# Kernel tuning notes

Measured on AMD Instinct MI355X. Metric: run time of the kernel, lower is better.

## Reference

```python
import jax, jax.numpy as jnp
import numpy as np

N = 50000        # n nodes (cells)
C = 1024         # common genes
H = 128          # edge_h_dim
HG = 128         # edge_hidden
E = 1600000      # edges (avg degree 32)
LAYERS = 2       # gnn_layers (unset in original __init__; fixed here)
EPS = 1e-8


def setup_inputs() -> dict:
    key = jax.random.key(0)
    ks = jax.random.split(key, 10)
    x_common = jax.random.normal(ks[0], (N, C), dtype=jnp.float32)
    src = jax.random.randint(ks[1], (E,), 0, N, dtype=jnp.int32)
    dst = jax.random.randint(ks[2], (E,), 0, N, dtype=jnp.int32)
    base_w = jax.random.uniform(ks[3], (E,), dtype=jnp.float32)
    # encoder params: Linear(C,H) -> ReLU -> Linear(H,H) -> ReLU
    W1 = jax.random.normal(ks[4], (C, H), dtype=jnp.float32) * 0.02
    b1 = jnp.zeros((H,), dtype=jnp.float32)
    W2 = jax.random.normal(ks[5], (H, H), dtype=jnp.float32) * 0.1
    b2 = jnp.zeros((H,), dtype=jnp.float32)
    # edge gate params: Linear(2H, HG) -> ReLU -> Linear(HG, 1)
    Wg1 = jax.random.normal(ks[6], (2 * H, HG), dtype=jnp.float32) * 0.1
    bg1 = jnp.zeros((HG,), dtype=jnp.float32)
    Wg2 = jax.random.normal(ks[7], (HG, 1), dtype=jnp.float32) * 0.1
    bg2 = jnp.full((1,), 2.0, dtype=jnp.float32)  # original init: bias=2.0
    # node reliability logits
    rho_raw = jax.random.normal(ks[8], (N,), dtype=jnp.float32) * 0.5
    return dict(x_common=x_common, src=src, dst=dst, base_w=base_w,
                W1=W1, b1=b1, W2=W2, b2=b2,
                Wg1=Wg1, bg1=bg1, Wg2=Wg2, bg2=bg2, rho_raw=rho_raw)


def reference(x_common, src, dst, base_w, W1, b1, W2, b2, Wg1, bg1, Wg2, bg2, rho_raw):
    # enc: [N, C] -> [N, H]
    h = jax.nn.relu(jax.nn.relu(x_common @ W1 + b1) @ W2 + b2)
    rho = jax.nn.sigmoid(rho_raw)                 # [N]
    rr = rho[src] * rho[dst]                      # [E] per-edge reliability factor
    for _ in range(LAYERS):
        h_src = h[src]                            # [E, H] gather
        h_dst = h[dst]                            # [E, H] gather
        z = jnp.concatenate([h_src, h_dst], axis=1)               # [E, 2H]
        gate = jax.nn.sigmoid(jax.nn.relu(z @ Wg1 + bg1) @ Wg2 + bg2)[:, 0]  # [E]
        w = base_w * gate * rr                    # [E]
        m = jax.ops.segment_sum(w[:, None] * h_src, dst, num_segments=N)     # [N, H]
        deg = jax.ops.segment_sum(w, dst, num_segments=N)                    # [N]
        h = m / (deg[:, None] + EPS)
    return h
```

## Files before the change

### kernel.cpp

```cpp
#include <hip/hip_runtime.h>
#include <stdint.h>

#define NN 50000
#define CC 1024
#define HH 128
#define EE 1600000
#define EPSV 1e-8f
#define NSTRIPE 8
#define STRIPE_N 6250
#define NBUCK (NN*NSTRIPE)
#define SCAN_BLKS 1563

typedef __attribute__((ext_vector_type(8))) short bf16x8;
typedef __attribute__((ext_vector_type(4))) float f32x4;
typedef __attribute__((ext_vector_type(2))) float f32x2;

__device__ __forceinline__ unsigned short f32_to_bf16(float f){
  union { float f; uint32_t u; } cv; cv.f = f;
  uint32_t u = cv.u;
  return (unsigned short)((u + 0x7FFFu + ((u >> 16) & 1u)) >> 16);
}
__device__ __forceinline__ float bf16lo_to_f32(uint32_t w){
  union { uint32_t u; float f; } cv; cv.u = w << 16; return cv.f;
}
__device__ __forceinline__ float bf16hi_to_f32(uint32_t w){
  union { uint32_t u; float f; } cv; cv.u = w & 0xFFFF0000u; return cv.f;
}

#define DPP_ADD(x, ctrl) ((x) + __int_as_float(__builtin_amdgcn_update_dpp(0, __float_as_int(x), (ctrl), 0xF, 0xF, true)))

#define GLOAD_LDS16(g, l) __builtin_amdgcn_global_load_lds( \
    (const __attribute__((address_space(1))) uint32_t*)(g), \
    (__attribute__((address_space(3))) uint32_t*)(l), 16, 0, 0)


__global__ __launch_bounds__(256) void k_prep_all(
    const float* __restrict__ W1, const float* __restrict__ W2,
    const float* __restrict__ Wg1,
    unsigned short* __restrict__ W1T, unsigned short* __restrict__ W2T,
    unsigned short* __restrict__ Wg1T){
  int idx = blockIdx.x*256 + threadIdx.x;
  if(idx < 131072){
    int n = idx >> 10, k = idx & 1023;
    W1T[idx] = f32_to_bf16(W1[k*128 + n]);
  } else if(idx < 131072 + 16384){
    int i = idx - 131072;
    int n = i >> 7, k = i & 127;
    W2T[i] = f32_to_bf16(W2[k*128 + n]);
  } else if(idx < 131072 + 16384 + 32768){
    int i = idx - 131072 - 16384;
    int c = i >> 7, k = i & 127;
    int row = (c < 128) ? k : (128 + k);
    int col = (c < 128) ? c : (c - 128);
    Wg1T[i] = f32_to_bf16(Wg1[row*128 + col]);
  }
}


__global__ __launch_bounds__(256) void k_hist(const int* __restrict__ src,
    const int* __restrict__ dst, int* __restrict__ counts,
    int* __restrict__ rank){
  int e = blockIdx.x*256 + threadIdx.x;
  if(e >= EE) return;
  int key = dst[e]*NSTRIPE + (int)((unsigned)src[e] / STRIPE_N);
  rank[e] = atomicAdd(&counts[key], 1);
}

__global__ __launch_bounds__(256) void k_scan1(const int* __restrict__ counts,
    int* __restrict__ lexcl, int* __restrict__ bsum){
  __shared__ int buf[256];
  const int t = threadIdx.x, i = blockIdx.x*256 + t;
  int v = (i < NBUCK) ? counts[i] : 0;
  buf[t] = v;
  __syncthreads();
  for(int off = 1; off < 256; off <<= 1){
    int add = (t >= off) ? buf[t-off] : 0;
    __syncthreads();
    buf[t] += add;
    __syncthreads();
  }
  if(i < NBUCK) lexcl[i] = buf[t] - v;
  if(t == 255) bsum[blockIdx.x] = buf[255];
}

__global__ __launch_bounds__(1024) void k_scan_mid(const int* __restrict__ bsum,
    int* __restrict__ bexcl){
  __shared__ int buf[1024];
  __shared__ int carry_s;
  const int t = threadIdx.x;
  if(t == 0) carry_s = 0;
  __syncthreads();
  for(int base = 0; base < SCAN_BLKS; base += 1024){
    int v = (base+t < SCAN_BLKS) ? bsum[base+t] : 0;
    buf[t] = v;
    __syncthreads();
    for(int off = 1; off < 1024; off <<= 1){
      int add = (t >= off) ? buf[t-off] : 0;
      __syncthreads();
      buf[t] += add;
      __syncthreads();
    }
    int carry = carry_s;
    if(base+t < SCAN_BLKS) bexcl[base+t] = carry + buf[t] - v;
    __syncthreads();
    if(t == 1023) carry_s = carry + buf[1023];
    __syncthreads();
  }
}

__global__ __launch_bounds__(256) void k_scan3(const int* __restrict__ lexcl,
    const int* __restrict__ bexcl, int* __restrict__ bptr){
  const int i = blockIdx.x*256 + threadIdx.x;
  if(i < NBUCK) bptr[i] = lexcl[i] + bexcl[blockIdx.x];
  if(i == 0) bptr[NBUCK] = EE;
}

__global__ __launch_bounds__(256) void k_fill(const int* __restrict__ src,
    const int* __restrict__ dst, const float* __restrict__ base_w,
    const float* __restrict__ rho_raw, const int* __restrict__ bptr,
    const int* __restrict__ rank, float2* __restrict__ scp){
  int e = blockIdx.x*256 + threadIdx.x;
  if(e >= EE) return;
  int s = src[e], d = dst[e];
  int key = d*NSTRIPE + (int)((unsigned)s / STRIPE_N);
  int p = bptr[key] + rank[e];
  float rs = 1.f/(1.f + __expf(-rho_raw[s]));
  float rd = 1.f/(1.f + __expf(-rho_raw[d]));
  scp[p] = make_float2(base_w[e]*rs*rd, __int_as_float(s));
}


__global__ __launch_bounds__(256) void k_enc1(
    const float* __restrict__ X, const unsigned short* __restrict__ W1T,
    const float* __restrict__ b1, unsigned short* __restrict__ h1)
{
  __shared__ __attribute__((aligned(16))) float          Af[2][64*32];
  __shared__ __attribute__((aligned(16))) unsigned short Bf[2][128*32];

  const int t = threadIdx.x, w = t >> 6, lane = t & 63;
  const int rowL = lane & 15, kq = lane >> 4;
  const int wm = w >> 1, wn = w & 1;
  const int row0 = blockIdx.x * 64;

  const int a_rl0 = w*16 + (lane >> 3);
  const int a_cl  = lane & 7;
  int agr0 = row0 + a_rl0;     if(agr0 >= NN) agr0 = NN-1;
  int agr1 = row0 + a_rl0 + 8; if(agr1 >= NN) agr1 = NN-1;
  const float* a_src0 = X + (size_t)agr0*1024 + (a_cl ^ (a_rl0 & 7))*4;
  const float* a_src1 = X + (size_t)agr1*1024 + (a_cl ^ ((a_rl0+8) & 7))*4;
  const int b_rl0 = w*32 + (lane >> 2);
  const int b_cl  = lane & 3;
  const int bkey0 = (b_rl0 ^ (b_rl0 >> 2)) & 3;
  const int bkey1 = ((b_rl0+16) ^ ((b_rl0+16) >> 2)) & 3;
  const unsigned short* b_src0 = W1T + (size_t)b_rl0*1024 + (b_cl ^ bkey0)*8;
  const unsigned short* b_src1 = W1T + (size_t)(b_rl0+16)*1024 + (b_cl ^ bkey1)*8;

  #define STAGE(buf, k0)  do{                                              \
    GLOAD_LDS16(a_src0 + (k0), &Af[buf][(w*16    )*32]);                   \
    GLOAD_LDS16(a_src1 + (k0), &Af[buf][(w*16 + 8)*32]);                   \
    GLOAD_LDS16(b_src0 + (k0), &Bf[buf][(w*32     )*32]);                  \
    GLOAD_LDS16(b_src1 + (k0), &Bf[buf][(w*32 + 16)*32]);                  \
  }while(0)

  f32x4 acc[2][4] = {};
  const int arow0 = wm*32 + rowL;
  const int akey  = rowL & 7;
  const int bkeyR = (rowL ^ (rowL >> 2)) & 3;

  auto COMPUTE = [&](const float* afb, const unsigned short* bfb){
    bf16x8 af[2];
    #pragma unroll
    for(int mf = 0; mf < 2; mf++){
      const int ar = arow0 + mf*16;
      f32x4 x0 = *(const f32x4*)&afb[ar*32 + (((2*kq  ) ^ akey) << 2)];
      f32x4 x1 = *(const f32x4*)&afb[ar*32 + (((2*kq+1) ^ akey) << 2)];
      union { bf16x8 v; unsigned short s[8]; } pk;
      #pragma unroll
      for(int j = 0; j < 4; j++){ pk.s[j] = f32_to_bf16(x0[j]); pk.s[4+j] = f32_to_bf16(x1[j]); }
      af[mf] = pk.v;
    }
    bf16x8 bfr[4];
    #pragma unroll
    for(int nf = 0; nf < 4; nf++){
      const int br = wn*64 + nf*16 + rowL;
      bfr[nf] = *(const bf16x8*)&bfb[br*32 + ((kq ^ bkeyR) << 3)];
    }
    #pragma unroll
    for(int mf = 0; mf < 2; mf++)
      #pragma unroll
      for(int nf = 0; nf < 4; nf++)
        acc[mf][nf] = __builtin_amdgcn_mfma_f32_16x16x32_bf16(af[mf], bfr[nf], acc[mf][nf], 0, 0, 0);
  };

  #define STEP(cbuf, sbuf, sk)  do{                                        \
    STAGE(sbuf, (sk)*32);                                                  \
    asm volatile("s_waitcnt vmcnt(4)" ::: "memory");                       \
    __builtin_amdgcn_s_barrier();                                          \
    __builtin_amdgcn_sched_barrier(0);                                     \
    COMPUTE(&Af[cbuf][0], &Bf[cbuf][0]);                                   \
    __builtin_amdgcn_s_barrier();                                          \
  }while(0)

  STAGE(0, 0);
  for(int tt = 0; tt < 30; tt += 2){
    STEP(0, 1, tt + 1);
    STEP(1, 0, tt + 2);
  }
  STEP(0, 1, 31);
  asm volatile("s_waitcnt vmcnt(0)" ::: "memory");
  __builtin_amdgcn_s_barrier();
  __builtin_amdgcn_sched_barrier(0);
  COMPUTE(&Af[1][0], &Bf[1][0]);
  #undef STEP
  #undef STAGE

  #pragma unroll
  for(int mf = 0; mf < 2; mf++){
    #pragma unroll
    for(int nf = 0; nf < 4; nf++){
      const int col = wn*64 + nf*16 + rowL;
      const float bv = b1[col];
      #pragma unroll
      for(int r = 0; r < 4; r++){
        const int gr = row0 + wm*32 + mf*16 + kq*4 + r;
        if(gr < NN) h1[(size_t)gr*128 + col] = f32_to_bf16(fmaxf(acc[mf][nf][r] + bv, 0.f));
      }
    }
  }
}


__device__ __forceinline__ void uv_phase2(
    const unsigned short* hs, const unsigned short* wgl, int row0, int wave, int lane,
    const float* __restrict__ bg1,
    unsigned short* __restrict__ UH, float* __restrict__ Vf)
{
  const int rowL = lane & 15, kq = lane >> 4;
  const int r = wave*16 + rowL;
  f32x4 acc[16] = {};
  #pragma unroll
  for(int ks = 0; ks < 4; ks++){
    const int kc = ks*4 + kq;
    bf16x8 a = *(const bf16x8*)&hs[r*128 + ((kc ^ (r & 15)) << 3)];
    #pragma unroll
    for(int nt = 0; nt < 16; nt++){
      bf16x8 b = *(const bf16x8*)&wgl[(nt*16 + rowL)*128 + ((kc ^ rowL) << 3)];
      acc[nt] = __builtin_amdgcn_mfma_f32_16x16x32_bf16(a, b, acc[nt], 0, 0, 0);
    }
  }
  #pragma unroll
  for(int nt = 0; nt < 16; nt++){
    const int col = nt*16 + rowL;
    #pragma unroll
    for(int rr = 0; rr < 4; rr++){
      const int gr = row0 + wave*16 + kq*4 + rr;
      if(gr < NN){
        if(col < 128) UH[(size_t)gr*256 + col] = f32_to_bf16(acc[nt][rr]);
        else          Vf[(size_t)gr*128 + col - 128] = acc[nt][rr] + bg1[col - 128];
      }
    }
  }
}


__global__ __launch_bounds__(256) void k_uvA(
    const unsigned short* __restrict__ h1, const unsigned short* __restrict__ W2T,
    const float* __restrict__ b2, const unsigned short* __restrict__ Wg1T,
    const float* __restrict__ bg1, unsigned short* __restrict__ UH,
    float* __restrict__ Vf)
{
  __shared__ __attribute__((aligned(16))) unsigned short hs[64*128];
  __shared__ __attribute__((aligned(16))) unsigned short wgl[256*128];
  const int t = threadIdx.x, wave = t >> 6, lane = t & 63;
  const int rowL = lane & 15, kq = lane >> 4;
  const int row0 = blockIdx.x*64;

  bf16x8 wreg[16];
  #pragma unroll
  for(int i = 0; i < 16; i++)
    wreg[i] = *(const bf16x8*)(Wg1T + (i*256 + t)*8);

  int ar = row0 + wave*16 + rowL; if(ar >= NN) ar = NN-1;
  f32x4 acc[8] = {};
  #pragma unroll
  for(int ks = 0; ks < 4; ks++){
    bf16x8 a = *(const bf16x8*)(h1 + (size_t)ar*128 + ks*32 + kq*8);
    #pragma unroll
    for(int nt = 0; nt < 8; nt++){
      bf16x8 b = *(const bf16x8*)(W2T + (nt*16 + rowL)*128 + ks*32 + kq*8);
      acc[nt] = __builtin_amdgcn_mfma_f32_16x16x32_bf16(a, b, acc[nt], 0, 0, 0);
    }
  }
  #pragma unroll
  for(int nt = 0; nt < 8; nt++){
    const int col = nt*16 + rowL;
    const float bv = b2[col];
    #pragma unroll
    for(int r = 0; r < 4; r++){
      const int rw = wave*16 + kq*4 + r;
      const unsigned short hv = f32_to_bf16(fmaxf(acc[nt][r] + bv, 0.f));
      hs[rw*128 + (((col >> 3) ^ (rw & 15)) << 3) + (col & 7)] = hv;
    }
  }
  #pragma unroll
  for(int i = 0; i < 16; i++){
    const int idx = i*256 + t, row = idx >> 4, c = idx & 15;
    *(bf16x8*)&wgl[row*128 + ((c ^ (row & 15)) << 3)] = wreg[i];
  }
  __syncthreads();
  {
    const int r = t >> 2, gr = row0 + r;
    if(gr < NN){
      #pragma unroll
      for(int j8 = 0; j8 < 4; j8++){
        const int chunk = (t & 3)*4 + j8;
        bf16x8 v = *(const bf16x8*)&hs[r*128 + ((chunk ^ (r & 15)) << 3)];
        *(bf16x8*)&UH[(size_t)gr*256 + 128 + chunk*8] = v;
      }
    }
  }
  uv_phase2(hs, wgl, row0, wave, lane, bg1, UH, Vf);
}


__global__ __launch_bounds__(256) void k_uvB(
    const float* __restrict__ hf, const unsigned short* __restrict__ Wg1T,
    const float* __restrict__ bg1, unsigned short* __restrict__ UH,
    float* __restrict__ Vf)
{
  __shared__ __attribute__((aligned(16))) unsigned short hs[64*128];
  __shared__ __attribute__((aligned(16))) unsigned short wgl[256*128];
  const int t = threadIdx.x, wave = t >> 6, lane = t & 63;
  const int row0 = blockIdx.x*64;

  bf16x8 wreg[16];
  #pragma unroll
  for(int i = 0; i < 16; i++)
    wreg[i] = *(const bf16x8*)(Wg1T + (i*256 + t)*8);

  {
    const int r = t >> 2, gr0 = row0 + r;
    const int gr = (gr0 < NN) ? gr0 : NN-1;
    const float* p = hf + (size_t)gr*128 + (t & 3)*32;
    #pragma unroll
    for(int j8 = 0; j8 < 4; j8++){
      f32x4 v0 = *(const f32x4*)(p + j8*8);
      f32x4 v1 = *(const f32x4*)(p + j8*8 + 4);
      union { bf16x8 v; unsigned short s[8]; } pk;
      #pragma unroll
      for(int j = 0; j < 4; j++){ pk.s[j] = f32_to_bf16(v0[j]); pk.s[4+j] = f32_to_bf16(v1[j]); }
      const int chunk = (t & 3)*4 + j8;
      *(bf16x8*)&hs[r*128 + ((chunk ^ (r & 15)) << 3)] = pk.v;
      if(gr0 < NN) *(bf16x8*)&UH[(size_t)gr0*256 + 128 + chunk*8] = pk.v;
    }
  }
  #pragma unroll
  for(int i = 0; i < 16; i++){
    const int idx = i*256 + t, row = idx >> 4, c = idx & 15;
    *(bf16x8*)&wgl[row*128 + ((c ^ (row & 15)) << 3)] = wreg[i];
  }
  __syncthreads();
  uv_phase2(hs, wgl, row0, wave, lane & 63, bg1, UH, Vf);
}


__global__ __launch_bounds__(256) void k_gate_agg(
    const unsigned short* __restrict__ UH, const float* __restrict__ Vf,
    const int* __restrict__ bptr, const float2* __restrict__ scp,
    const float* __restrict__ Wg2, const float* __restrict__ bg2p,
    float* __restrict__ out_f32)
{
  __shared__ float2 ws_s[4][64];
  const int wv = threadIdx.x >> 6, lane = threadIdx.x & 63;
  const int gw = blockIdx.x*4 + wv;
  if(gw >= NN) return;
  const int eq = lane >> 4, li = lane & 15;

  f32x4 va = *(const f32x4*)(Vf + (size_t)gw*128 + li*8);
  f32x4 vb = *(const f32x4*)(Vf + (size_t)gw*128 + li*8 + 4);
  f32x4 wa = *(const f32x4*)(Wg2 + li*8);
  f32x4 wb = *(const f32x4*)(Wg2 + li*8 + 4);
  const float vch[8]  = {va[0],va[1],va[2],va[3],vb[0],vb[1],vb[2],vb[3]};
  const float w2ch[8] = {wa[0],wa[1],wa[2],wa[3],wb[0],wb[1],wb[2],wb[3]};
  const float bg2v = bg2p[0];

  const int beg = bptr[gw*NSTRIPE], end = bptr[gw*NSTRIPE + NSTRIPE];
  float a0 = 0.f, a1 = 0.f, wsum = 0.f;

  for(int base = beg; base < end; base += 64){
    const int nb = min(64, end - base);

    float2 sc_c0, sc_c1; bf16x8 u_c0, u_c1;
    {
      const int i0 = (eq     < nb) ? eq     : 0;
      const int i1 = (4 + eq < nb) ? 4 + eq : 0;
      sc_c0 = scp[base + i0]; sc_c1 = scp[base + i1];
      u_c0 = *(const bf16x8*)&UH[(uint32_t)__float_as_int(sc_c0.y)*256u + li*8];
      u_c1 = *(const bf16x8*)&UH[(uint32_t)__float_as_int(sc_c1.y)*256u + li*8];
    }
    for(int q = 0; q < nb; q += 8){
      float2 sc_n0 = sc_c0, sc_n1 = sc_c1; bf16x8 u_n0 = u_c0, u_n1 = u_c1;
      if(q + 8 < nb){
        const int i0 = (q + 8  + eq < nb) ? q + 8  + eq : 0;
        const int i1 = (q + 12 + eq < nb) ? q + 12 + eq : 0;
        sc_n0 = scp[base + i0]; sc_n1 = scp[base + i1];
        u_n0 = *(const bf16x8*)&UH[(uint32_t)__float_as_int(sc_n0.y)*256u + li*8];
        u_n1 = *(const bf16x8*)&UH[(uint32_t)__float_as_int(sc_n1.y)*256u + li*8];
      }
      {
        union { bf16x8 v; uint32_t u32[4]; } uu; uu.v = u_c0;
        float tacc = 0.f;
        #pragma unroll
        for(int p = 0; p < 4; p++){
          const uint32_t w2b = uu.u32[p];
          tacc += fmaxf(bf16lo_to_f32(w2b) + vch[2*p],   0.f) * w2ch[2*p];
          tacc += fmaxf(bf16hi_to_f32(w2b) + vch[2*p+1], 0.f) * w2ch[2*p+1];
        }
        tacc = DPP_ADD(tacc, 0xB1);
        tacc = DPP_ADD(tacc, 0x4E);
        tacc = DPP_ADD(tacc, 0x141);
        tacc = DPP_ADD(tacc, 0x140);
        const float g = 1.f/(1.f + __expf(-(tacc + bg2v)));
        const int idx = q + eq;
        if(li == 0 && idx < nb) ws_s[wv][idx] = make_float2(sc_c0.x*g, sc_c0.y);
      }
      {
        union { bf16x8 v; uint32_t u32[4]; } uu; uu.v = u_c1;
        float tacc = 0.f;
        #pragma unroll
        for(int p = 0; p < 4; p++){
          const uint32_t w2b = uu.u32[p];
          tacc += fmaxf(bf16lo_to_f32(w2b) + vch[2*p],   0.f) * w2ch[2*p];
          tacc += fmaxf(bf16hi_to_f32(w2b) + vch[2*p+1], 0.f) * w2ch[2*p+1];
        }
        tacc = DPP_ADD(tacc, 0xB1);
        tacc = DPP_ADD(tacc, 0x4E);
        tacc = DPP_ADD(tacc, 0x141);
        tacc = DPP_ADD(tacc, 0x140);
        const float g = 1.f/(1.f + __expf(-(tacc + bg2v)));
        const int idx = q + 4 + eq;
        if(li == 0 && idx < nb) ws_s[wv][idx] = make_float2(sc_c1.x*g, sc_c1.y);
      }
      sc_c0 = sc_n0; sc_c1 = sc_n1; u_c0 = u_n0; u_c1 = u_n1;
    }

    #pragma unroll 8
    for(int j = 0; j < nb; j++){
      const float2 p = ws_s[wv][j];
      const float w  = p.x;
      const uint32_t s = (uint32_t)__float_as_int(p.y);
      const uint32_t hw = *(const uint32_t*)&UH[s*256u + 128u + lane*2];
      a0 += w*bf16lo_to_f32(hw);
      a1 += w*bf16hi_to_f32(hw);
      wsum += w;
    }
  }
  const float inv = 1.f/(wsum + EPSV);
  const size_t o = (size_t)gw*128 + lane*2;
  *(f32x2*)&out_f32[o] = (f32x2){a0*inv, a1*inv};
}


extern "C" void kernel_launch(void* const* d_in, const int* in_sizes, int n_in,
                              void* d_out, int out_size, void* d_ws, size_t ws_size,
                              hipStream_t stream) {
  (void)in_sizes; (void)n_in; (void)out_size; (void)ws_size;
  const float* X      = (const float*)d_in[0];
  const int*   src    = (const int*)d_in[1];
  const int*   dst    = (const int*)d_in[2];
  const float* base_w = (const float*)d_in[3];
  const float* W1     = (const float*)d_in[4];
  const float* b1     = (const float*)d_in[5];
  const float* W2     = (const float*)d_in[6];
  const float* b2     = (const float*)d_in[7];
  const float* Wg1    = (const float*)d_in[8];
  const float* bg1    = (const float*)d_in[9];
  const float* Wg2    = (const float*)d_in[10];
  const float* bg2    = (const float*)d_in[11];
  const float* rho    = (const float*)d_in[12];

  char* ws = (char*)d_ws;
  size_t off = 0;
  auto alloc = [&](size_t bytes)->char*{ char* p = ws + off; off += (bytes + 255) & ~(size_t)255; return p; };
  unsigned short* W1T      = (unsigned short*)alloc((size_t)1024*128*2);
  unsigned short* W2T      = (unsigned short*)alloc((size_t)128*128*2);
  unsigned short* Wg1T     = (unsigned short*)alloc((size_t)256*128*2);
  int*            rank     = (int*)alloc((size_t)EE*4);
  float2*         scp      = (float2*)alloc((size_t)EE*8);
  int*            bptr     = (int*)alloc((size_t)(NBUCK+1)*4);
  int*            counts   = (int*)alloc((size_t)NBUCK*4);
  int*            lexcl    = (int*)alloc((size_t)NBUCK*4);
  int*            bsum     = (int*)alloc((size_t)SCAN_BLKS*4);
  int*            bexcl    = (int*)alloc((size_t)SCAN_BLKS*4);
  unsigned short* h1       = (unsigned short*)alloc((size_t)NN*128*2);
  unsigned short* UH       = (unsigned short*)alloc((size_t)NN*256*2);
  float*          Vf       = (float*)alloc((size_t)NN*128*4);
  float*          hf_B     = (float*)alloc((size_t)NN*128*4);

  hipMemsetAsync(counts, 0, (size_t)NBUCK*4, stream);
  k_prep_all<<<704, 256, 0, stream>>>(W1, W2, Wg1, W1T, W2T, Wg1T);
  k_hist<<<EE/256, 256, 0, stream>>>(src, dst, counts, rank);
  k_scan1<<<SCAN_BLKS, 256, 0, stream>>>(counts, lexcl, bsum);
  k_scan_mid<<<1, 1024, 0, stream>>>(bsum, bexcl);
  k_scan3<<<SCAN_BLKS, 256, 0, stream>>>(lexcl, bexcl, bptr);
  k_fill<<<EE/256, 256, 0, stream>>>(src, dst, base_w, rho, bptr, rank, scp);

  k_enc1<<<782, 256, 0, stream>>>(X, W1T, b1, h1);

  k_uvA<<<782, 256, 0, stream>>>(h1, W2T, b2, Wg1T, bg1, UH, Vf);
  k_gate_agg<<<12500, 256, 0, stream>>>(UH, Vf, bptr, scp, Wg2, bg2, hf_B);
  k_uvB<<<782, 256, 0, stream>>>(hf_B, Wg1T, bg1, UH, Vf);
  k_gate_agg<<<12500, 256, 0, stream>>>(UH, Vf, bptr, scp, Wg2, bg2, (float*)d_out);
}
```

Baseline: 498.7 us.

## Co-schedule edge histogram and fill with encoder GEMM kernels via block partitioning

Merges the edge histogram kernel into the first encoder GEMM launch and the CSR fill kernel into the second-stage (uvA) launch by giving extra blocks an edge-processing role. Independent memory-bound edge work now runs concurrently with the compute-heavy GEMM blocks, and two launches are removed. In exchange, the edge blocks reserve the GEMM kernels' full shared-memory footprint, which can lower their occupancy, and the GEMM blocks' scheduling order relative to the edge blocks changes.

Result: faster. 443.4 us (-11.1%).

```diff
diff --git a/kernel.cpp b/kernel.cpp
--- a/kernel.cpp
+++ b/kernel.cpp
@@ -10,6 +10,9 @@
 #define STRIPE_N 6250
 #define NBUCK (NN*NSTRIPE)
 #define SCAN_BLKS 1563
+#define ENC_BLKS 782
+#define UV_BLKS 782
+#define EDGE_BLKS (EE/256)
 
 typedef __attribute__((ext_vector_type(8))) short bf16x8;
 typedef __attribute__((ext_vector_type(4))) float f32x4;
@@ -57,14 +60,116 @@
 }
 
 
-__global__ __launch_bounds__(256) void k_hist(const int* __restrict__ src,
-    const int* __restrict__ dst, int* __restrict__ counts,
-    int* __restrict__ rank){
-  int e = blockIdx.x*256 + threadIdx.x;
-  if(e >= EE) return;
-  int key = dst[e]*NSTRIPE + (int)((unsigned)src[e] / STRIPE_N);
-  rank[e] = atomicAdd(&counts[key], 1);
-}
+__global__ __launch_bounds__(256) void k_enc1_hist(
+    const float* __restrict__ X, const unsigned short* __restrict__ W1T,
+    const float* __restrict__ b1, unsigned short* __restrict__ h1,
+    const int* __restrict__ src, const int* __restrict__ dst,
+    int* __restrict__ counts, int* __restrict__ rank)
+{
+  __shared__ __attribute__((aligned(16))) float          Af[2][64*32];
+  __shared__ __attribute__((aligned(16))) unsigned short Bf[2][128*32];
+
+  if(blockIdx.x >= ENC_BLKS){
+    int e = (blockIdx.x - ENC_BLKS)*256 + threadIdx.x;
+    if(e < EE){
+      int key = dst[e]*NSTRIPE + (int)((unsigned)src[e] / STRIPE_N);
+      rank[e] = atomicAdd(&counts[key], 1);
+    }
+    return;
+  }
+
+  const int t = threadIdx.x, w = t >> 6, lane = t & 63;
+  const int rowL = lane & 15, kq = lane >> 4;
+  const int wm = w >> 1, wn = w & 1;
+  const int row0 = blockIdx.x * 64;
+
+  const int a_rl0 = w*16 + (lane >> 3);
+  const int a_cl  = lane & 7;
+  int agr0 = row0 + a_rl0;     if(agr0 >= NN) agr0 = NN-1;
+  int agr1 = row0 + a_rl0 + 8; if(agr1 >= NN) agr1 = NN-1;
+  const float* a_src0 = X + (size_t)agr0*1024 + (a_cl ^ (a_rl0 & 7))*4;
+  const float* a_src1 = X + (size_t)agr1*1024 + (a_cl ^ ((a_rl0+8) & 7))*4;
+  const int b_rl0 = w*32 + (lane >> 2);
+  const int b_cl  = lane & 3;
+  const int bkey0 = (b_rl0 ^ (b_rl0 >> 2)) & 3;
+  const int bkey1 = ((b_rl0+16) ^ ((b_rl0+16) >> 2)) & 3;
+  const unsigned short* b_src0 = W1T + (size_t)b_rl0*1024 + (b_cl ^ bkey0)*8;
+  const unsigned short* b_src1 = W1T + (size_t)(b_rl0+16)*1024 + (b_cl ^ bkey1)*8;
+
+  #define STAGE(buf, k0)  do{                                              \
+    GLOAD_LDS16(a_src0 + (k0), &Af[buf][(w*16    )*32]);                   \
+    GLOAD_LDS16(a_src1 + (k0), &Af[buf][(w*16 + 8)*32]);                   \
+    GLOAD_LDS16(b_src0 + (k0), &Bf[buf][(w*32     )*32]);                  \
+    GLOAD_LDS16(b_src1 + (k0), &Bf[buf][(w*32 + 16)*32]);                  \
+  }while(0)
+
+  f32x4 acc[2][4] = {};
+  const int arow0 = wm*32 + rowL;
+  const int akey  = rowL & 7;
+  const int bkeyR = (rowL ^ (rowL >> 2)) & 3;
+
+  auto COMPUTE = [&](const float* afb, const unsigned short* bfb){
+    bf16x8 af[2];
+    #pragma unroll
+    for(int mf = 0; mf < 2; mf++){
+      const int ar = arow0 + mf*16;
+      f32x4 x0 = *(const f32x4*)&afb[ar*32 + (((2*kq  ) ^ akey) << 2)];
+      f32x4 x1 = *(const f32x4*)&afb[ar*32 + (((2*kq+1) ^ akey) << 2)];
+      union { bf16x8 v; unsigned short s[8]; } pk;
+      #pragma unroll
+      for(int j = 0; j < 4; j++){ pk.s[j] = f32_to_bf16(x0[j]); pk.s[4+j] = f32_to_bf16(x1[j]); }
+      af[mf] = pk.v;
+    }
+    bf16x8 bfr[4];
+    #pragma unroll
+    for(int nf = 0; nf < 4; nf++){
+      const int br = wn*64 + nf*16 + rowL;
+      bfr[nf] = *(const bf16x8*)&bfb[br*32 + ((kq ^ bkeyR) << 3)];
+    }
+    #pragma unroll
+    for(int mf = 0; mf < 2; mf++)
+      #pragma unroll
+      for(int nf = 0; nf < 4; nf++)
+        acc[mf][nf] = __builtin_amdgcn_mfma_f32_16x16x32_bf16(af[mf], bfr[nf], acc[mf][nf], 0, 0, 0);
+  };
+
+  #define STEP(cbuf, sbuf, sk)  do{                                        \
+    STAGE(sbuf, (sk)*32);                                                  \
+    asm volatile("s_waitcnt vmcnt(4)" ::: "memory");                       \
+    __builtin_amdgcn_s_barrier();                                          \
+    __builtin_amdgcn_sched_barrier(0);                                     \
+    COMPUTE(&Af[cbuf][0], &Bf[cbuf][0]);                                   \
+    __builtin_amdgcn_s_barrier();                                          \
+  }while(0)
+
+  STAGE(0, 0);
+  for(int tt = 0; tt < 30; tt += 2){
+    STEP(0, 1, tt + 1);
+    STEP(1, 0, tt + 2);
+  }
+  STEP(0, 1, 31);
+  asm volatile("s_waitcnt vmcnt(0)" ::: "memory");
+  __builtin_amdgcn_s_barrier();
+  __builtin_amdgcn_sched_barrier(0);
+  COMPUTE(&Af[1][0], &Bf[1][0]);
+  #undef STEP
+  #undef STAGE
+
+  #pragma unroll
+  for(int mf = 0; mf < 2; mf++){
+    #pragma unroll
+    for(int nf = 0; nf < 4; nf++){
+      const int col = wn*64 + nf*16 + rowL;
+      const float bv = b1[col];
+      #pragma unroll
+      for(int r = 0; r < 4; r++){
+        const int gr = row0 + wm*32 + mf*16 + kq*4 + r;
+        if(gr < NN) h1[(size_t)gr*128 + col] = f32_to_bf16(fmaxf(acc[mf][nf][r] + bv, 0.f));
+      }
+    }
+  }
+}
+
 
 __global__ __launch_bounds__(256) void k_scan1(const int* __restrict__ counts,
     int* __restrict__ lexcl, int* __restrict__ bsum){
@@ -115,120 +220,6 @@
   if(i == 0) bptr[NBUCK] = EE;
 }
 
-__global__ __launch_bounds__(256) void k_fill(const int* __restrict__ src,
-    const int* __restrict__ dst, const float* __restrict__ base_w,
-    const float* __restrict__ rho_raw, const int* __restrict__ bptr,
-    const int* __restrict__ rank, float2* __restrict__ scp){
-  int e = blockIdx.x*256 + threadIdx.x;
-  if(e >= EE) return;
-  int s = src[e], d = dst[e];
-  int key = d*NSTRIPE + (int)((unsigned)s / STRIPE_N);
-  int p = bptr[key] + rank[e];
-  float rs = 1.f/(1.f + __expf(-rho_raw[s]));
-  float rd = 1.f/(1.f + __expf(-rho_raw[d]));
-  scp[p] = make_float2(base_w[e]*rs*rd, __int_as_float(s));
-}
-
-
-__global__ __launch_bounds__(256) void k_enc1(
-    const float* __restrict__ X, const unsigned short* __restrict__ W1T,
-    const float* __restrict__ b1, unsigned short* __restrict__ h1)
-{
-  __shared__ __attribute__((aligned(16))) float          Af[2][64*32];
-  __shared__ __attribute__((aligned(16))) unsigned short Bf[2][128*32];
-
-  const int t = threadIdx.x, w = t >> 6, lane = t & 63;
-  const int rowL = lane & 15, kq = lane >> 4;
-  const int wm = w >> 1, wn = w & 1;
-  const int row0 = blockIdx.x * 64;
-
-  const int a_rl0 = w*16 + (lane >> 3);
-  const int a_cl  = lane & 7;
-  int agr0 = row0 + a_rl0;     if(agr0 >= NN) agr0 = NN-1;
-  int agr1 = row0 + a_rl0 + 8; if(agr1 >= NN) agr1 = NN-1;
-  const float* a_src0 = X + (size_t)agr0*1024 + (a_cl ^ (a_rl0 & 7))*4;
-  const float* a_src1 = X + (size_t)agr1*1024 + (a_cl ^ ((a_rl0+8) & 7))*4;
-  const int b_rl0 = w*32 + (lane >> 2);
-  const int b_cl  = lane & 3;
-  const int bkey0 = (b_rl0 ^ (b_rl0 >> 2)) & 3;
-  const int bkey1 = ((b_rl0+16) ^ ((b_rl0+16) >> 2)) & 3;
-  const unsigned short* b_src0 = W1T + (size_t)b_rl0*1024 + (b_cl ^ bkey0)*8;
-  const unsigned short* b_src1 = W1T + (size_t)(b_rl0+16)*1024 + (b_cl ^ bkey1)*8;
-
-  #define STAGE(buf, k0)  do{                                              \
-    GLOAD_LDS16(a_src0 + (k0), &Af[buf][(w*16    )*32]);                   \
-    GLOAD_LDS16(a_src1 + (k0), &Af[buf][(w*16 + 8)*32]);                   \
-    GLOAD_LDS16(b_src0 + (k0), &Bf[buf][(w*32     )*32]);                  \
-    GLOAD_LDS16(b_src1 + (k0), &Bf[buf][(w*32 + 16)*32]);                  \
-  }while(0)
-
-  f32x4 acc[2][4] = {};
-  const int arow0 = wm*32 + rowL;
-  const int akey  = rowL & 7;
-  const int bkeyR = (rowL ^ (rowL >> 2)) & 3;
-
-  auto COMPUTE = [&](const float* afb, const unsigned short* bfb){
-    bf16x8 af[2];
-    #pragma unroll
-    for(int mf = 0; mf < 2; mf++){
-      const int ar = arow0 + mf*16;
-      f32x4 x0 = *(const f32x4*)&afb[ar*32 + (((2*kq  ) ^ akey) << 2)];
-      f32x4 x1 = *(const f32x4*)&afb[ar*32 + (((2*kq+1) ^ akey) << 2)];
-      union { bf16x8 v; unsigned short s[8]; } pk;
-      #pragma unroll
-      for(int j = 0; j < 4; j++){ pk.s[j] = f32_to_bf16(x0[j]); pk.s[4+j] = f32_to_bf16(x1[j]); }
-      af[mf] = pk.v;
-    }
-    bf16x8 bfr[4];
-    #pragma unroll
-    for(int nf = 0; nf < 4; nf++){
-      const int br = wn*64 + nf*16 + rowL;
-      bfr[nf] = *(const bf16x8*)&bfb[br*32 + ((kq ^ bkeyR) << 3)];
-    }
-    #pragma unroll
-    for(int mf = 0; mf < 2; mf++)
-      #pragma unroll
-      for(int nf = 0; nf < 4; nf++)
-        acc[mf][nf] = __builtin_amdgcn_mfma_f32_16x16x32_bf16(af[mf], bfr[nf], acc[mf][nf], 0, 0, 0);
-  };
-
-  #define STEP(cbuf, sbuf, sk)  do{                                        \
-    STAGE(sbuf, (sk)*32);                                                  \
-    asm volatile("s_waitcnt vmcnt(4)" ::: "memory");                       \
-    __builtin_amdgcn_s_barrier();                                          \
-    __builtin_amdgcn_sched_barrier(0);                                     \
-    COMPUTE(&Af[cbuf][0], &Bf[cbuf][0]);                                   \
-    __builtin_amdgcn_s_barrier();                                          \
-  }while(0)
-
-  STAGE(0, 0);
-  for(int tt = 0; tt < 30; tt += 2){
-    STEP(0, 1, tt + 1);
-    STEP(1, 0, tt + 2);
-  }
-  STEP(0, 1, 31);
-  asm volatile("s_waitcnt vmcnt(0)" ::: "memory");
-  __builtin_amdgcn_s_barrier();
-  __builtin_amdgcn_sched_barrier(0);
-  COMPUTE(&Af[1][0], &Bf[1][0]);
-  #undef STEP
-  #undef STAGE
-
-  #pragma unroll
-  for(int mf = 0; mf < 2; mf++){
-    #pragma unroll
-    for(int nf = 0; nf < 4; nf++){
-      const int col = wn*64 + nf*16 + rowL;
-      const float bv = b1[col];
-      #pragma unroll
-      for(int r = 0; r < 4; r++){
-        const int gr = row0 + wm*32 + mf*16 + kq*4 + r;
-        if(gr < NN) h1[(size_t)gr*128 + col] = f32_to_bf16(fmaxf(acc[mf][nf][r] + bv, 0.f));
-      }
-    }
-  }
-}
-
 
 __device__ __forceinline__ void uv_phase2(
     const unsigned short* hs, const unsigned short* wgl, int row0, int wave, int lane,
@@ -263,14 +254,32 @@
 }
 
 
-__global__ __launch_bounds__(256) void k_uvA(
+__global__ __launch_bounds__(256) void k_uvA_fill(
     const unsigned short* __restrict__ h1, const unsigned short* __restrict__ W2T,
     const float* __restrict__ b2, const unsigned short* __restrict__ Wg1T,
     const float* __restrict__ bg1, unsigned short* __restrict__ UH,
-    float* __restrict__ Vf)
+    float* __restrict__ Vf,
+    const int* __restrict__ src, const int* __restrict__ dst,
+    const float* __restrict__ base_w, const float* __restrict__ rho_raw,
+    const int* __restrict__ bptr, const int* __restrict__ rank,
+    float2* __restrict__ scp)
 {
   __shared__ __attribute__((aligned(16))) unsigned short hs[64*128];
   __shared__ __attribute__((aligned(16))) unsigned short wgl[256*128];
+
+  if(blockIdx.x >= UV_BLKS){
+    int e = (blockIdx.x - UV_BLKS)*256 + threadIdx.x;
+    if(e < EE){
+      int s = src[e], d = dst[e];
+      int key = d*NSTRIPE + (int)((unsigned)s / STRIPE_N);
+      int p = bptr[key] + rank[e];
+      float rs = 1.f/(1.f + __expf(-rho_raw[s]));
+      float rd = 1.f/(1.f + __expf(-rho_raw[d]));
+      scp[p] = make_float2(base_w[e]*rs*rd, __int_as_float(s));
+    }
+    return;
+  }
+
   const int t = threadIdx.x, wave = t >> 6, lane = t & 63;
   const int rowL = lane & 15, kq = lane >> 4;
   const int row0 = blockIdx.x*64;
@@ -499,15 +508,17 @@
 
   hipMemsetAsync(counts, 0, (size_t)NBUCK*4, stream);
   k_prep_all<<<704, 256, 0, stream>>>(W1, W2, Wg1, W1T, W2T, Wg1T);
-  k_hist<<<EE/256, 256, 0, stream>>>(src, dst, counts, rank);
+
+  k_enc1_hist<<<ENC_BLKS + EDGE_BLKS, 256, 0, stream>>>(
+      X, W1T, b1, h1, src, dst, counts, rank);
+
   k_scan1<<<SCAN_BLKS, 256, 0, stream>>>(counts, lexcl, bsum);
   k_scan_mid<<<1, 1024, 0, stream>>>(bsum, bexcl);
   k_scan3<<<SCAN_BLKS, 256, 0, stream>>>(lexcl, bexcl, bptr);
-  k_fill<<<EE/256, 256, 0, stream>>>(src, dst, base_w, rho, bptr, rank, scp);
-
-  k_enc1<<<782, 256, 0, stream>>>(X, W1T, b1, h1);
-
-  k_uvA<<<782, 256, 0, stream>>>(h1, W2T, b2, Wg1T, bg1, UH, Vf);
+
+  k_uvA_fill<<<UV_BLKS + EDGE_BLKS, 256, 0, stream>>>(
+      h1, W2T, b2, Wg1T, bg1, UH, Vf, src, dst, base_w, rho, bptr, rank, scp);
+
   k_gate_agg<<<12500, 256, 0, stream>>>(UH, Vf, bptr, scp, Wg2, bg2, hf_B);
   k_uvB<<<782, 256, 0, stream>>>(hf_B, Wg1T, bg1, UH, Vf);
   k_gate_agg<<<12500, 256, 0, stream>>>(UH, Vf, bptr, scp, Wg2, bg2, (float*)d_out);
```
